# Performance work log

Measured on AMD Instinct MI355X. Metric: run time of the kernel, lower is better.

Reference implementation:

```python
import jax, jax.numpy as jnp
import numpy as np

C_IN, C_OUT = 256, 128

def setup_inputs() -> dict:
    key = jax.random.key(0)
    k1, k2, k3, k4, k5, k6 = jax.random.split(key, 6)
    B, H, W = 8, 64, 64
    p = jax.random.normal(k1, (B, C_IN, H, W), dtype=jnp.float32)
    b = jax.random.normal(k2, (B, C_IN, H, W), dtype=jnp.float32)
    # 1x1 conv weights (Conv2d with kernel 1 == pointwise matmul) + biases
    sq = 1.0 / np.sqrt(C_IN)
    Wq = jax.random.uniform(k3, (C_OUT, C_IN), jnp.float32, -sq, sq)
    bq = jax.random.uniform(k4, (C_OUT,), jnp.float32, -sq, sq)
    Wk = jax.random.uniform(k5, (C_OUT, C_IN), jnp.float32, -sq, sq)
    bk = jax.random.uniform(k6, (C_OUT,), jnp.float32, -sq, sq)
    return {"p": p, "b": b, "Wq": Wq, "bq": bq, "Wk": Wk, "bk": bk}

def reference(p, b, Wq, bq, Wk, bk):
    B, C, H, W = p.shape
    N = H * W
    # 1x1 convs -> flatten spatial dim to N
    q = jnp.einsum('bchw,oc->bhwo', p, Wq) + bq          # [B,H,W,Co]
    q = q.reshape(B, N, -1).astype(jnp.float32)           # [B,N,Co] (query permuted)
    k = jnp.einsum('bchw,oc->bohw', b, Wk) + bk[None, :, None, None]
    k = k.reshape(B, -1, N).astype(jnp.float32)           # [B,Co,N]
    energy = jnp.einsum('bnc,bcm->bnm', q, k)             # [B,N,N] unscaled
    attention = jax.nn.softmax(energy, axis=-1)           # softmax over keys
    value = b.reshape(B, C, N)                            # [B,C,N]
    out = jnp.einsum('bnm,bcm->bcn', attention, value)    # [B,C,N]
    return out.reshape(B, C, H, W)
```

## Files before the change

### kernel.cpp

```cpp
#include <hip/hip_runtime.h>
#include <hip/hip_bf16.h>
#include <math.h>


#define B_   8
#define CIN  256
#define COUT 128
#define NN   4096

typedef _Float16 half8  __attribute__((ext_vector_type(8)));
typedef short    short8 __attribute__((ext_vector_type(8)));
typedef float    f32x4  __attribute__((ext_vector_type(4)));

#define LOG2E 1.44269504088896340736f

__device__ __forceinline__ unsigned short f2h(float f) {
    union { _Float16 h; unsigned short u; } v; v.h = (_Float16)f;
    return v.u;
}
__device__ __forceinline__ unsigned int cvt_pk_bf16(float lo, float hi) {
    unsigned int r;
    asm("v_cvt_pk_bf16_f32 %0, %1, %2" : "=v"(r) : "v"(lo), "v"(hi));
    return r;
}
__device__ __forceinline__ unsigned int pkrtz(float lo, float hi) {
    typedef __fp16 fp16x2 __attribute__((ext_vector_type(2)));
    union { fp16x2 h; unsigned int u; } c;
    c.h = __builtin_amdgcn_cvt_pkrtz(lo, hi);
    return c.u;
}
__device__ __forceinline__ float dpp_xor1(float x) {
    union { float f; int i; } u; u.f = x;
    u.i = __builtin_amdgcn_mov_dpp(u.i, 0xB1, 0xF, 0xF, true);
    return u.f;
}
__device__ __forceinline__ void dma16(void* lds, const void* g) {
    __builtin_amdgcn_global_load_lds(
        (const __attribute__((address_space(1))) unsigned int*)g,
        (__attribute__((address_space(3))) unsigned int*)lds,
        16, 0, 0);
}

__global__ __launch_bounds__(256) void cvt_w(const float* __restrict__ Wq,
                                             const float* __restrict__ Wk,
                                             const float* __restrict__ bq,
                                             _Float16* __restrict__ Whq,
                                             _Float16* __restrict__ Whk,
                                             float* __restrict__ bqs) {
    const int bx = blockIdx.x, t = threadIdx.x;
    const int isK = (bx >= 32);
    const float* src = isK ? Wk : Wq;
    _Float16* dst = isK ? Whk : Whq;
    const float scale = isK ? 1.0f : LOG2E;
    const int idx = (bx & 31) * 256 + t;
    float4 v = ((const float4*)src)[idx];
    unsigned long long pk = (unsigned long long)f2h(v.x * scale)
                          | ((unsigned long long)f2h(v.y * scale) << 16)
                          | ((unsigned long long)f2h(v.z * scale) << 32)
                          | ((unsigned long long)f2h(v.w * scale) << 48);
    ((unsigned long long*)dst)[idx] = pk;
    if (bx == 0 && t < COUT) bqs[t] = bq[t] * LOG2E;
}

__global__ __launch_bounds__(256, 3) void proj_all(
        const float* __restrict__ P,
        const float* __restrict__ Bv,
        const _Float16* __restrict__ Whq,
        const _Float16* __restrict__ Whk,
        const float* __restrict__ bqs,
        const float* __restrict__ bk,
        _Float16* __restrict__ Qh,
        _Float16* __restrict__ Ktt,
        unsigned short* __restrict__ Vb)
{
    __shared__ __align__(16) unsigned short T[64 * 136];
    const int bx = blockIdx.x;
    const int isK = bx >> 9;
    const int bl  = bx & 511;
    const int b   = bl >> 6, n0 = (bl & 63) << 6;
    const int t   = threadIdx.x;

    const float*    X    = isK ? Bv  : P;
    const _Float16* Wh   = isK ? Whk : Whq;
    const float*    bias = isK ? bk  : bqs;

    if (isK) {
        const int cr = t >> 2;
        const int nch = (t & 3) << 4;
#pragma unroll
        for (int it = 0; it < 4; ++it) {
            const int c = it * 64 + cr;
            const float* src = X + ((size_t)(b * CIN + c) * NN + n0 + nch);
            unsigned int o2[8];
#pragma unroll
            for (int k = 0; k < 4; ++k) {
                float4 f = *(const float4*)(src + k * 4);
                o2[k * 2]     = cvt_pk_bf16(f.x, f.y);
                o2[k * 2 + 1] = cvt_pk_bf16(f.z, f.w);
            }
            unsigned short* dst = Vb + (size_t)(b * CIN + c) * NN + n0 + nch;
            *(int4*)dst = *(int4*)&o2[0];
            *(int4*)(dst + 8) = *(int4*)&o2[4];
        }
    }

    const int w = t >> 6, lane = t & 63, l15 = lane & 15, quad = lane >> 4, q8 = quad * 8;

    half8 a[8];
    {
        const float* Xa = X + ((size_t)(b * CIN + q8) * NN) + n0 + w * 16 + l15;
#pragma unroll
        for (int s = 0; s < 8; ++s) {
            const float* xs = Xa + (size_t)s * 32 * NN;
            float av[8];
#pragma unroll
            for (int j = 0; j < 8; ++j) av[j] = xs[(size_t)j * NN];
            union { half8 h; unsigned int u[4]; } af;
#pragma unroll
            for (int j = 0; j < 4; ++j) af.u[j] = pkrtz(av[2 * j], av[2 * j + 1]);
            a[s] = af.h;
        }
    }

    f32x4 D[8];
#pragma unroll
    for (int og = 0; og < 8; ++og) D[og] = (f32x4){0.f, 0.f, 0.f, 0.f};
    const _Float16* wbase = Wh + (size_t)l15 * CIN + q8;
#pragma unroll
    for (int s = 0; s < 8; ++s) {
        const _Float16* wp = wbase + s * 32;
#pragma unroll
        for (int og = 0; og < 8; ++og) {
            half8 wfv = *(const half8*)(wp + og * 16 * CIN);
            D[og] = __builtin_amdgcn_mfma_f32_16x16x32_f16(a[s], wfv, D[og], 0, 0, 0);
        }
    }

    const int nrow = w * 16 + quad * 4;
    if (isK) {
#pragma unroll
        for (int og = 0; og < 8; ++og) {
            const int o = og * 16 + l15;
            const float bo = bias[o];
            const int c = o >> 3, j = o & 7;
            const int sw = (c & 7) << 2;
#pragma unroll
            for (int r2 = 0; r2 < 4; ++r2) {
                const int n = nrow + r2;
                const int tl = n >> 5, m = n & 31;
                T[tl * 4096 + (c * 32 + ((m + sw) & 31)) * 8 + j] = f2h(D[og][r2] + bo);
            }
        }
        __syncthreads();
        _Float16* dstk = Ktt + ((size_t)(b * 128 + (n0 >> 5)) * 4096 + t * 32);
        const unsigned short* srck = T + t * 32;
#pragma unroll
        for (int k = 0; k < 4; ++k)
            ((int4*)dstk)[k] = ((const int4*)srck)[k];
    } else {
#pragma unroll
        for (int og = 0; og < 8; ++og) {
            const int o = og * 16 + l15;
            const float bo = bias[o];
#pragma unroll
            for (int r2 = 0; r2 < 4; ++r2)
                T[(nrow + r2) * 136 + o] = f2h(D[og][r2] + bo);
        }
        __syncthreads();
        const int n = t >> 2, seg = t & 3;
        const unsigned short* srcp = T + n * 136 + seg * 32;
        _Float16* dstp = Qh + ((size_t)(b * NN + n0 + n) * COUT + seg * 32);
#pragma unroll
        for (int k = 0; k < 4; ++k)
            ((int4*)dstp)[k] = ((const int4*)srcp)[k];
    }
}

__global__ __launch_bounds__(256, 2) void flash_kernel(const _Float16* __restrict__ Q,
                                                       const _Float16* __restrict__ Ktt,
                                                       const unsigned short* __restrict__ V,
                                                       float* __restrict__ out) {
    __shared__ __align__(16) _Float16       K0sh[32 * 128];
    __shared__ __align__(16) _Float16       K1sh[32 * 128];
    __shared__ __align__(16) unsigned short V0sh[256 * 32];
    __shared__ __align__(16) unsigned short V1sh[256 * 32];
    __shared__ __align__(16) unsigned short V2sh[256 * 32];
    __shared__ __align__(16) unsigned short P0sh[64 * 40];
    __shared__ __align__(16) unsigned short P1sh[64 * 40];
    __shared__ __align__(16) float          Lsh[64];

    const int bx   = blockIdx.x;
    const int b    = bx >> 6;
    const int q0   = (bx & 63) << 6;
    const int t    = threadIdx.x;
    const int w    = t >> 6;
    const int lane = t & 63;
    const int l15  = lane & 15;
    const int quad = lane >> 4;
    const int q8   = quad * 8;

    const _Float16* Qg = Q + (size_t)b * NN * COUT;
    const _Float16* Kb = Ktt + (size_t)b * 128 * 4096;
    const unsigned short* Vg = V + (size_t)b * CIN * NN;

    half8 Qf[4];
    {
        const _Float16* qr = Qg + (size_t)(q0 + w * 16 + l15) * COUT;
#pragma unroll
        for (int s = 0; s < 4; ++s)
            Qf[s] = *(const half8*)(qr + s * 32 + q8);
    }

    f32x4 O[16];
#pragma unroll
    for (int i = 0; i < 16; ++i) O[i] = (f32x4){0.f, 0.f, 0.f, 0.f};
    float lsum[4] = {0.f, 0.f, 0.f, 0.f};

    const int vmq   = ((lane & 3) - ((lane >> 3) & 3)) & 3;
    const int vcrow = lane >> 2;
    const int vslot = (quad + (l15 >> 1)) & 3;

    auto issueK = [&](int kt, _Float16* Kd) {
        const _Float16* gk = Kb + (size_t)kt * 4096;
        dma16(Kd + (w * 2 + 0) * 512, gk + (w * 2 + 0) * 512 + lane * 8);
        dma16(Kd + (w * 2 + 1) * 512, gk + (w * 2 + 1) * 512 + lane * 8);
    };
    auto issueV = [&](int kt, unsigned short* Vd) {
        const int k0 = kt << 5;
#pragma unroll
        for (int i = 0; i < 4; ++i) {
            const int cc = (w * 4 + i) * 16 + vcrow;
            dma16(Vd + (w * 4 + i) * 512,
                  Vg + (size_t)cc * NN + k0 + vmq * 8);
        }
    };

    auto halfstep = [&](int kt, const _Float16* Kc, _Float16* Kn,
                        const unsigned short* Va, unsigned short* Vn2,
                        unsigned short* Pc) {
        if (kt + 1 < 128) issueK(kt + 1, Kn);

        f32x4 S0 = {0.f, 0.f, 0.f, 0.f}, S1 = {0.f, 0.f, 0.f, 0.f};
        __builtin_amdgcn_s_setprio(1);
#pragma unroll
        for (int s = 0; s < 4; ++s) {
            const int kc = 4 * s + quad;
            const int sw = (kc & 7) << 2;
            const int x0 = (l15 + sw) & 31;
            half8 kf0 = *(const half8*)(Kc + (kc * 32 + x0) * 8);
            half8 kf1 = *(const half8*)(Kc + (kc * 32 + (x0 ^ 16)) * 8);
            S0 = __builtin_amdgcn_mfma_f32_16x16x32_f16(Qf[s], kf0, S0, 0, 0, 0);
            S1 = __builtin_amdgcn_mfma_f32_16x16x32_f16(Qf[s], kf1, S1, 0, 0, 0);
        }
        __builtin_amdgcn_s_setprio(0);

        f32x4 E0, E1;
#pragma unroll
        for (int r = 0; r < 4; ++r) {
            E0[r] = exp2f(S0[r]);
            E1[r] = exp2f(S1[r]);
            lsum[r] += E0[r] + E1[r];
        }
        {
            f32x4 P0, P1;
#pragma unroll
            for (int r = 0; r < 4; ++r) { P0[r] = dpp_xor1(E0[r]); P1[r] = dpp_xor1(E1[r]); }
            const int odd = l15 & 1;
            unsigned short* wp0 = Pc + w * 640
                                + (((quad << 2) + (odd << 1)) * 40) + (l15 & ~1);
            unsigned int pk0 = cvt_pk_bf16(odd ? P0[2] : E0[0], odd ? E0[2] : P0[0]);
            unsigned int pk1 = cvt_pk_bf16(odd ? P0[3] : E0[1], odd ? E0[3] : P0[1]);
            unsigned int pk2 = cvt_pk_bf16(odd ? P1[2] : E1[0], odd ? E1[2] : P1[0]);
            unsigned int pk3 = cvt_pk_bf16(odd ? P1[3] : E1[1], odd ? E1[3] : P1[1]);
            *(unsigned int*)&wp0[0]  = pk0;
            *(unsigned int*)&wp0[40] = pk1;
            *(unsigned int*)&wp0[16] = pk2;
            *(unsigned int*)&wp0[56] = pk3;
        }

        __syncthreads();

        if (kt + 2 < 128) issueV(kt + 2, Vn2);

        {
            short8 pf[4];
#pragma unroll
            for (int ni = 0; ni < 4; ++ni)
                pf[ni] = *(const short8*)(Pc + (ni * 16 + l15) * 40 + q8);
            const unsigned short* vb = Va + (w * 64 + l15) * 32 + vslot * 8;
            __builtin_amdgcn_s_setprio(1);
#pragma unroll
            for (int cj = 0; cj < 4; ++cj) {
                short8 vf = *(const short8*)(vb + cj * 512);
#pragma unroll
                for (int ni = 0; ni < 4; ++ni)
                    O[ni * 4 + cj] = __builtin_amdgcn_mfma_f32_16x16x32_bf16(pf[ni], vf, O[ni * 4 + cj], 0, 0, 0);
            }
            __builtin_amdgcn_s_setprio(0);
        }
    };

    issueK(0, K0sh);
    issueV(0, V0sh);
    issueV(1, V1sh);
    __syncthreads();

    _Float16*       Kc = K0sh; _Float16*       Kn = K1sh;
    unsigned short* Va = V0sh; unsigned short* Vm = V1sh; unsigned short* Vn2 = V2sh;
    unsigned short* Pc = P0sh; unsigned short* Pn = P1sh;
#pragma unroll 1
    for (int kt = 0; kt < 128; ++kt) {
        halfstep(kt, Kc, Kn, Va, Vn2, Pc);
        _Float16* tk = Kc; Kc = Kn; Kn = tk;
        unsigned short* tv = Va; Va = Vm; Vm = Vn2; Vn2 = tv;
        unsigned short* tp = Pc; Pc = Pn; Pn = tp;
    }

#pragma unroll
    for (int r = 0; r < 4; ++r) {
        float s = lsum[r];
        s += __shfl_xor(s, 1);
        s += __shfl_xor(s, 2);
        s += __shfl_xor(s, 4);
        s += __shfl_xor(s, 8);
        if (l15 == 0) Lsh[w * 16 + (quad << 2) + r] = s;
    }
    __syncthreads();
    float* ob = out + (size_t)b * CIN * NN + q0;
#pragma unroll
    for (int ni = 0; ni < 4; ++ni) {
        const f32x4 lv = *(const f32x4*)&Lsh[ni * 16 + (quad << 2)];
        f32x4 linv;
#pragma unroll
        for (int r = 0; r < 4; ++r) linv[r] = 1.0f / lv[r];
        const int nb = ni * 16 + (quad << 2);
#pragma unroll
        for (int cj = 0; cj < 4; ++cj) {
            const int c = w * 64 + cj * 16 + l15;
            f32x4 val = O[ni * 4 + cj];
#pragma unroll
            for (int r = 0; r < 4; ++r) val[r] *= linv[r];
            *(f32x4*)(ob + (size_t)c * NN + nb) = val;
        }
    }
}

extern "C" void kernel_launch(void* const* d_in, const int* in_sizes, int n_in,
                              void* d_out, int out_size, void* d_ws, size_t ws_size,
                              hipStream_t stream) {
    const float* p  = (const float*)d_in[0];
    const float* bv = (const float*)d_in[1];
    const float* Wq = (const float*)d_in[2];
    const float* bq = (const float*)d_in[3];
    const float* Wk = (const float*)d_in[4];
    const float* bk = (const float*)d_in[5];
    float* outp = (float*)d_out;

    char* ws = (char*)d_ws;
    const size_t szQ = (size_t)B_ * NN * COUT * 2;
    const size_t szV = (size_t)B_ * NN * CIN * 2;
    const size_t szW = (size_t)COUT * CIN * 2;
    _Float16*       Qh  = (_Float16*)ws;
    _Float16*       Ktt = (_Float16*)(ws + szQ);
    unsigned short* Vb  = (unsigned short*)(ws + 2 * szQ);
    _Float16*       Whq = (_Float16*)(ws + 2 * szQ + szV);
    _Float16*       Whk = (_Float16*)(ws + 2 * szQ + szV + szW);
    float*          bqs = (float*)(ws + 2 * szQ + szV + 2 * szW);

    cvt_w<<<64, 256, 0, stream>>>(Wq, Wk, bq, Whq, Whk, bqs);
    proj_all<<<1024, 256, 0, stream>>>(p, bv, Whq, Whk, bqs, bk, Qh, Ktt, Vb);
    flash_kernel<<<512, 256, 0, stream>>>(Qh, Ktt, Vb, outp);
}
```

Measured before the change: 281.4 us.

## Fuse Q projection into flash kernel and split K/V prep kernel

Moves the query 1x1-conv projection out of the projection kernel and into the flash-attention prologue. Each flash block now computes its own 64 query rows from the fp32 input with MFMA and stages them through reused shared memory. This removes the Qh workspace round trip and halves the prep kernel's grid to K/V only. In exchange the flash kernel prologue grows, it reads fp32 P directly, and its shared memory becomes one explicit 76KB buffer, which could affect occupancy.

Result: faster. 275.8 us (-2.0%).

```diff
diff --git a/kernel.cpp b/kernel.cpp
--- a/kernel.cpp
+++ b/kernel.cpp
@@ -62,35 +62,25 @@
     if (bx == 0 && t < COUT) bqs[t] = bq[t] * LOG2E;
 }
 
-__global__ __launch_bounds__(256, 3) void proj_all(
-        const float* __restrict__ P,
+__global__ __launch_bounds__(256) void kv_prep(
         const float* __restrict__ Bv,
-        const _Float16* __restrict__ Whq,
         const _Float16* __restrict__ Whk,
-        const float* __restrict__ bqs,
         const float* __restrict__ bk,
-        _Float16* __restrict__ Qh,
         _Float16* __restrict__ Ktt,
         unsigned short* __restrict__ Vb)
 {
     __shared__ __align__(16) unsigned short T[64 * 136];
     const int bx = blockIdx.x;
-    const int isK = bx >> 9;
-    const int bl  = bx & 511;
-    const int b   = bl >> 6, n0 = (bl & 63) << 6;
-    const int t   = threadIdx.x;
-
-    const float*    X    = isK ? Bv  : P;
-    const _Float16* Wh   = isK ? Whk : Whq;
-    const float*    bias = isK ? bk  : bqs;
-
-    if (isK) {
+    const int b  = bx >> 6, n0 = (bx & 63) << 6;
+    const int t  = threadIdx.x;
+
+    {
         const int cr = t >> 2;
         const int nch = (t & 3) << 4;
 #pragma unroll
         for (int it = 0; it < 4; ++it) {
             const int c = it * 64 + cr;
-            const float* src = X + ((size_t)(b * CIN + c) * NN + n0 + nch);
+            const float* src = Bv + ((size_t)(b * CIN + c) * NN + n0 + nch);
             unsigned int o2[8];
 #pragma unroll
             for (int k = 0; k < 4; ++k) {
@@ -108,7 +98,7 @@
 
     half8 a[8];
     {
-        const float* Xa = X + ((size_t)(b * CIN + q8) * NN) + n0 + w * 16 + l15;
+        const float* Xa = Bv + ((size_t)(b * CIN + q8) * NN) + n0 + w * 16 + l15;
 #pragma unroll
         for (int s = 0; s < 8; ++s) {
             const float* xs = Xa + (size_t)s * 32 * NN;
@@ -125,7 +115,7 @@
     f32x4 D[8];
 #pragma unroll
     for (int og = 0; og < 8; ++og) D[og] = (f32x4){0.f, 0.f, 0.f, 0.f};
-    const _Float16* wbase = Wh + (size_t)l15 * CIN + q8;
+    const _Float16* wbase = Whk + (size_t)l15 * CIN + q8;
 #pragma unroll
     for (int s = 0; s < 8; ++s) {
         const _Float16* wp = wbase + s * 32;
@@ -137,57 +127,43 @@
     }
 
     const int nrow = w * 16 + quad * 4;
-    if (isK) {
-#pragma unroll
-        for (int og = 0; og < 8; ++og) {
-            const int o = og * 16 + l15;
-            const float bo = bias[o];
-            const int c = o >> 3, j = o & 7;
-            const int sw = (c & 7) << 2;
-#pragma unroll
-            for (int r2 = 0; r2 < 4; ++r2) {
-                const int n = nrow + r2;
-                const int tl = n >> 5, m = n & 31;
-                T[tl * 4096 + (c * 32 + ((m + sw) & 31)) * 8 + j] = f2h(D[og][r2] + bo);
-            }
-        }
-        __syncthreads();
-        _Float16* dstk = Ktt + ((size_t)(b * 128 + (n0 >> 5)) * 4096 + t * 32);
-        const unsigned short* srck = T + t * 32;
-#pragma unroll
-        for (int k = 0; k < 4; ++k)
-            ((int4*)dstk)[k] = ((const int4*)srck)[k];
-    } else {
-#pragma unroll
-        for (int og = 0; og < 8; ++og) {
-            const int o = og * 16 + l15;
-            const float bo = bias[o];
-#pragma unroll
-            for (int r2 = 0; r2 < 4; ++r2)
-                T[(nrow + r2) * 136 + o] = f2h(D[og][r2] + bo);
-        }
-        __syncthreads();
-        const int n = t >> 2, seg = t & 3;
-        const unsigned short* srcp = T + n * 136 + seg * 32;
-        _Float16* dstp = Qh + ((size_t)(b * NN + n0 + n) * COUT + seg * 32);
-#pragma unroll
-        for (int k = 0; k < 4; ++k)
-            ((int4*)dstp)[k] = ((const int4*)srcp)[k];
-    }
-}
-
-__global__ __launch_bounds__(256, 2) void flash_kernel(const _Float16* __restrict__ Q,
+#pragma unroll
+    for (int og = 0; og < 8; ++og) {
+        const int o = og * 16 + l15;
+        const float bo = bk[o];
+        const int c = o >> 3, j = o & 7;
+        const int sw = (c & 7) << 2;
+#pragma unroll
+        for (int r2 = 0; r2 < 4; ++r2) {
+            const int n = nrow + r2;
+            const int tl = n >> 5, m = n & 31;
+            T[tl * 4096 + (c * 32 + ((m + sw) & 31)) * 8 + j] = f2h(D[og][r2] + bo);
+        }
+    }
+    __syncthreads();
+    _Float16* dstk = Ktt + ((size_t)(b * 128 + (n0 >> 5)) * 4096 + t * 32);
+    const unsigned short* srck = T + t * 32;
+#pragma unroll
+    for (int k = 0; k < 4; ++k)
+        ((int4*)dstk)[k] = ((const int4*)srck)[k];
+}
+
+__global__ __launch_bounds__(256, 2) void flash_kernel(const float* __restrict__ Pin,
+                                                       const _Float16* __restrict__ Whq,
+                                                       const float* __restrict__ bqs,
                                                        const _Float16* __restrict__ Ktt,
                                                        const unsigned short* __restrict__ V,
                                                        float* __restrict__ out) {
-    __shared__ __align__(16) _Float16       K0sh[32 * 128];
-    __shared__ __align__(16) _Float16       K1sh[32 * 128];
-    __shared__ __align__(16) unsigned short V0sh[256 * 32];
-    __shared__ __align__(16) unsigned short V1sh[256 * 32];
-    __shared__ __align__(16) unsigned short V2sh[256 * 32];
-    __shared__ __align__(16) unsigned short P0sh[64 * 40];
-    __shared__ __align__(16) unsigned short P1sh[64 * 40];
-    __shared__ __align__(16) float          Lsh[64];
+    __shared__ __align__(16) char SH[76032];
+    _Float16*       K0sh = (_Float16*)(SH);
+    _Float16*       K1sh = (_Float16*)(SH + 8192);
+    unsigned short* V0sh = (unsigned short*)(SH + 16384);
+    unsigned short* V1sh = (unsigned short*)(SH + 32768);
+    unsigned short* V2sh = (unsigned short*)(SH + 49152);
+    unsigned short* P0sh = (unsigned short*)(SH + 65536);
+    unsigned short* P1sh = (unsigned short*)(SH + 70656);
+    float*          Lsh  = (float*)(SH + 75776);
+    unsigned short* T    = (unsigned short*)SH;
 
     const int bx   = blockIdx.x;
     const int b    = bx >> 6;
@@ -199,16 +175,51 @@
     const int quad = lane >> 4;
     const int q8   = quad * 8;
 
-    const _Float16* Qg = Q + (size_t)b * NN * COUT;
     const _Float16* Kb = Ktt + (size_t)b * 128 * 4096;
     const unsigned short* Vg = V + (size_t)b * CIN * NN;
 
     half8 Qf[4];
     {
-        const _Float16* qr = Qg + (size_t)(q0 + w * 16 + l15) * COUT;
+        half8 a[8];
+        const float* Xa = Pin + ((size_t)(b * CIN + q8) * NN) + q0 + w * 16 + l15;
+#pragma unroll
+        for (int s = 0; s < 8; ++s) {
+            const float* xs = Xa + (size_t)s * 32 * NN;
+            float av[8];
+#pragma unroll
+            for (int j = 0; j < 8; ++j) av[j] = xs[(size_t)j * NN];
+            union { half8 h; unsigned int u[4]; } af;
+#pragma unroll
+            for (int j = 0; j < 4; ++j) af.u[j] = pkrtz(av[2 * j], av[2 * j + 1]);
+            a[s] = af.h;
+        }
+        f32x4 D[8];
+#pragma unroll
+        for (int og = 0; og < 8; ++og) D[og] = (f32x4){0.f, 0.f, 0.f, 0.f};
+        const _Float16* wbase = Whq + (size_t)l15 * CIN + q8;
+#pragma unroll
+        for (int s = 0; s < 8; ++s) {
+            const _Float16* wp = wbase + s * 32;
+#pragma unroll
+            for (int og = 0; og < 8; ++og) {
+                half8 wfv = *(const half8*)(wp + og * 16 * CIN);
+                D[og] = __builtin_amdgcn_mfma_f32_16x16x32_f16(a[s], wfv, D[og], 0, 0, 0);
+            }
+        }
+        const int nrow = w * 16 + quad * 4;
+#pragma unroll
+        for (int og = 0; og < 8; ++og) {
+            const int o = og * 16 + l15;
+            const float bo = bqs[o];
+#pragma unroll
+            for (int r2 = 0; r2 < 4; ++r2)
+                T[(nrow + r2) * 136 + o] = f2h(D[og][r2] + bo);
+        }
+        __syncthreads();
 #pragma unroll
         for (int s = 0; s < 4; ++s)
-            Qf[s] = *(const half8*)(qr + s * 32 + q8);
+            Qf[s] = *(const half8*)&T[(w * 16 + l15) * 136 + s * 32 + q8];
+        __syncthreads();
     }
 
     f32x4 O[16];
@@ -357,17 +368,16 @@
     float* outp = (float*)d_out;
 
     char* ws = (char*)d_ws;
-    const size_t szQ = (size_t)B_ * NN * COUT * 2;
+    const size_t szK = (size_t)B_ * NN * COUT * 2;
     const size_t szV = (size_t)B_ * NN * CIN * 2;
     const size_t szW = (size_t)COUT * CIN * 2;
-    _Float16*       Qh  = (_Float16*)ws;
-    _Float16*       Ktt = (_Float16*)(ws + szQ);
-    unsigned short* Vb  = (unsigned short*)(ws + 2 * szQ);
-    _Float16*       Whq = (_Float16*)(ws + 2 * szQ + szV);
-    _Float16*       Whk = (_Float16*)(ws + 2 * szQ + szV + szW);
-    float*          bqs = (float*)(ws + 2 * szQ + szV + 2 * szW);
+    _Float16*       Ktt = (_Float16*)ws;
+    unsigned short* Vb  = (unsigned short*)(ws + szK);
+    _Float16*       Whq = (_Float16*)(ws + szK + szV);
+    _Float16*       Whk = (_Float16*)(ws + szK + szV + szW);
+    float*          bqs = (float*)(ws + szK + szV + 2 * szW);
 
     cvt_w<<<64, 256, 0, stream>>>(Wq, Wk, bq, Whq, Whk, bqs);
-    proj_all<<<1024, 256, 0, stream>>>(p, bv, Whq, Whk, bqs, bk, Qh, Ktt, Vb);
-    flash_kernel<<<512, 256, 0, stream>>>(Qh, Ktt, Vb, outp);
-}
+    kv_prep<<<512, 256, 0, stream>>>(bv, Whk, bk, Ktt, Vb);
+    flash_kernel<<<512, 256, 0, stream>>>(p, Whq, bqs, Ktt, Vb, outp);
+}
```
